# Performance work log

Hardware: AMD Instinct MI355X
Metric: run time of the kernel (lower is better)

Reference implementation:

```python
import jax, jax.numpy as jnp
import numpy as np

BATCH = 32768
NUM_CLASSES = 1024  # balanced binary hierarchy => 10 levels, 1023 internal nodes


def setup_inputs() -> dict:
    key = jax.random.key(0)
    outputs = jax.random.normal(key, (BATCH, NUM_CLASSES), dtype=jnp.float32)
    return {"outputs": outputs}


def reference(outputs) -> jnp.ndarray:
    """SoftEmbeddedDecisionRules.forward for a balanced binary hierarchy.

    For every internal node: child logit = mean of raw logits over the child's
    leaf (class) set, softmax over the node's children, then multiply each
    class's running probability by the prob of the branch containing it.
    With a balanced binary tree over C classes, level l has 2^l nodes, each
    child covering a contiguous block of C / 2^(l+1) classes, so the per-node
    Python loop of the original collapses into one reshape+mean+softmax per
    level (log2(C) fused passes total).
    """
    B, C = outputs.shape
    depth = C.bit_length() - 1  # log2(C), static
    class_probs = jnp.ones((B, C), dtype=outputs.dtype)
    for level in range(depth):
        n_nodes = 1 << level
        seg = C // (2 * n_nodes)  # classes per child subtree
        # node logits: mean of raw logits over each child's class block
        node_logits = outputs.reshape(B, n_nodes, 2, seg).mean(axis=-1)  # [B, n, 2]
        probs = jax.nn.softmax(node_logits, axis=-1)  # softmax over children
        # scatter-multiply child prob onto every class in that child's subtree
        expanded = jnp.broadcast_to(probs[..., None], (B, n_nodes, 2, seg)).reshape(B, C)
        class_probs = class_probs * expanded
    return class_probs
```

## Files before the change

kernel.cpp:

```cpp
#include <hip/hip_runtime.h>


#define C 1024

typedef float f4 __attribute__((ext_vector_type(4)));

__device__ __forceinline__ float sigd(float d) {
    return 1.0f / (1.0f + __expf(d));
}

__global__ __launch_bounds__(256) void hier_softmax_kernel(
    const float* __restrict__ in, float* __restrict__ out, int B) {
    const int lane = threadIdx.x & 63;
    const int waveId = (blockIdx.x * blockDim.x + threadIdx.x) >> 6;
    const int nWaves = (gridDim.x * blockDim.x) >> 6;

    for (int row = waveId; row < B; row += nWaves) {
        const f4* __restrict__ rowp = (const f4*)(in + (size_t)row * C);

        f4 v[4];
#pragma unroll
        for (int q = 0; q < 4; ++q) v[q] = rowp[q * 64 + lane];

        float pA[4], pB[4], p8[4], S[4], common[4];
#pragma unroll
        for (int q = 0; q < 4; ++q) {
            pA[q] = sigd(v[q].y - v[q].x);
            pB[q] = sigd(v[q].w - v[q].z);
            const float s2a = v[q].x + v[q].y;
            const float s2b = v[q].z + v[q].w;
            p8[q] = sigd((s2b - s2a) * 0.5f);
            S[q] = s2a + s2b;
            common[q] = 1.0f;
        }

        float inv = 0.25f;
#pragma unroll
        for (int m = 1; m <= 32; m <<= 1) {
#pragma unroll
            for (int q = 0; q < 4; ++q) {
                const float sib = __shfl_xor(S[q], m, 64);
                common[q] *= sigd((sib - S[q]) * inv);
                S[q] += sib;
            }
            inv *= 0.5f;
        }
        const float topL = sigd(((S[2] + S[3]) - (S[0] + S[1])) * (1.0f / 512.0f));
        const float pq01 = sigd((S[1] - S[0]) * (1.0f / 256.0f));
        const float pq23 = sigd((S[3] - S[2]) * (1.0f / 256.0f));
        const float lvl01[4] = {topL * pq01, topL * (1.0f - pq01),
                                (1.0f - topL) * pq23, (1.0f - topL) * (1.0f - pq23)};

        f4* __restrict__ orow = (f4*)(out + (size_t)row * C);
#pragma unroll
        for (int q = 0; q < 4; ++q) {
            const float cm = common[q] * lvl01[q];
            const float cl = cm * p8[q];
            const float cr = cm * (1.0f - p8[q]);
            f4 o;
            o.x = cl * pA[q];
            o.y = cl * (1.0f - pA[q]);
            o.z = cr * pB[q];
            o.w = cr * (1.0f - pB[q]);
            __builtin_nontemporal_store(o, orow + q * 64 + lane);
        }
    }
}

extern "C" void kernel_launch(void* const* d_in, const int* in_sizes, int n_in,
                              void* d_out, int out_size, void* d_ws, size_t ws_size,
                              hipStream_t stream) {
    const float* in = (const float*)d_in[0];
    float* out = (float*)d_out;
    const int B = in_sizes[0] / C;
    hier_softmax_kernel<<<2048, 256, 0, stream>>>(in, out, B);
}
```

Baseline: 231.5 us.

## Give each lane a contiguous 16-float block and prefetch the next row

Each lane now loads 16 contiguous floats (four adjacent float4s) instead of strided float4s. The lower four tree levels are then resolved inside the lane, so each row needs a single 6-step shuffle reduction instead of four. The next row's data is loaded before the current row is computed, so memory latency overlaps with compute, and the launch bounds request 4 waves per SIMD. The 64-byte-per-lane access pattern may coalesce worse than the previous lane-strided float4 loads, and the prefetch buffer raises register use.

Result: slower. 363.7 us (+57.1%).

```diff
diff --git a/kernel.cpp b/kernel.cpp
--- a/kernel.cpp
+++ b/kernel.cpp
@@ -9,61 +9,98 @@
     return 1.0f / (1.0f + __expf(d));
 }
 
-__global__ __launch_bounds__(256) void hier_softmax_kernel(
+__global__ __launch_bounds__(256, 4) void hier_softmax_kernel(
     const float* __restrict__ in, float* __restrict__ out, int B) {
     const int lane = threadIdx.x & 63;
     const int waveId = (blockIdx.x * blockDim.x + threadIdx.x) >> 6;
     const int nWaves = (gridDim.x * blockDim.x) >> 6;
 
-    for (int row = waveId; row < B; row += nWaves) {
-        const f4* __restrict__ rowp = (const f4*)(in + (size_t)row * C);
+    int row = waveId;
+    if (row >= B) return;
 
-        f4 v[4];
+    f4 v[4];
+    {
+        const f4* rowp = (const f4*)(in + (size_t)row * C);
 #pragma unroll
-        for (int q = 0; q < 4; ++q) v[q] = rowp[q * 64 + lane];
+        for (int j = 0; j < 4; ++j) v[j] = rowp[lane * 4 + j];
+    }
 
-        float pA[4], pB[4], p8[4], S[4], common[4];
+    while (row < B) {
+        const int nrow = row + nWaves;
+        f4 vn[4];
+        if (nrow < B) {
+            const f4* np = (const f4*)(in + (size_t)nrow * C);
 #pragma unroll
-        for (int q = 0; q < 4; ++q) {
-            pA[q] = sigd(v[q].y - v[q].x);
-            pB[q] = sigd(v[q].w - v[q].z);
-            const float s2a = v[q].x + v[q].y;
-            const float s2b = v[q].z + v[q].w;
-            p8[q] = sigd((s2b - s2a) * 0.5f);
-            S[q] = s2a + s2b;
-            common[q] = 1.0f;
+            for (int j = 0; j < 4; ++j) vn[j] = np[lane * 4 + j];
         }
 
-        float inv = 0.25f;
+        float x[16];
+#pragma unroll
+        for (int j = 0; j < 4; ++j) {
+            x[4 * j + 0] = v[j].x; x[4 * j + 1] = v[j].y;
+            x[4 * j + 2] = v[j].z; x[4 * j + 3] = v[j].w;
+        }
+
+        float p1[8], s2[8];
+#pragma unroll
+        for (int k = 0; k < 8; ++k) {
+            p1[k] = sigd(x[2 * k + 1] - x[2 * k]);
+            s2[k] = x[2 * k] + x[2 * k + 1];
+        }
+        float p2[4], s4[4];
+#pragma unroll
+        for (int k = 0; k < 4; ++k) {
+            p2[k] = sigd((s2[2 * k + 1] - s2[2 * k]) * 0.5f);
+            s4[k] = s2[2 * k] + s2[2 * k + 1];
+        }
+        float p4[2], s8[2];
+#pragma unroll
+        for (int k = 0; k < 2; ++k) {
+            p4[k] = sigd((s4[2 * k + 1] - s4[2 * k]) * 0.25f);
+            s8[k] = s4[2 * k] + s4[2 * k + 1];
+        }
+        const float p8 = sigd((s8[1] - s8[0]) * 0.125f);
+        float S = s8[0] + s8[1];
+
+        float common = 1.0f;
+        float inv = 0.0625f;
 #pragma unroll
         for (int m = 1; m <= 32; m <<= 1) {
-#pragma unroll
-            for (int q = 0; q < 4; ++q) {
-                const float sib = __shfl_xor(S[q], m, 64);
-                common[q] *= sigd((sib - S[q]) * inv);
-                S[q] += sib;
-            }
+            const float sib = __shfl_xor(S, m, 64);
+            common *= sigd((sib - S) * inv);
+            S += sib;
             inv *= 0.5f;
         }
-        const float topL = sigd(((S[2] + S[3]) - (S[0] + S[1])) * (1.0f / 512.0f));
-        const float pq01 = sigd((S[1] - S[0]) * (1.0f / 256.0f));
-        const float pq23 = sigd((S[3] - S[2]) * (1.0f / 256.0f));
-        const float lvl01[4] = {topL * pq01, topL * (1.0f - pq01),
-                                (1.0f - topL) * pq23, (1.0f - topL) * (1.0f - pq23)};
 
-        f4* __restrict__ orow = (f4*)(out + (size_t)row * C);
+        float c8[2], c4[4], c2[8];
+        c8[0] = common * p8;
+        c8[1] = common - c8[0];
 #pragma unroll
-        for (int q = 0; q < 4; ++q) {
-            const float cm = common[q] * lvl01[q];
-            const float cl = cm * p8[q];
-            const float cr = cm * (1.0f - p8[q]);
+        for (int k = 0; k < 2; ++k) {
+            c4[2 * k] = c8[k] * p4[k];
+            c4[2 * k + 1] = c8[k] - c4[2 * k];
+        }
+#pragma unroll
+        for (int k = 0; k < 4; ++k) {
+            c2[2 * k] = c4[k] * p2[k];
+            c2[2 * k + 1] = c4[k] - c2[2 * k];
+        }
+
+        f4* orow = (f4*)(out + (size_t)row * C);
+#pragma unroll
+        for (int j = 0; j < 4; ++j) {
+            const int k0 = 2 * j, k1 = 2 * j + 1;
             f4 o;
-            o.x = cl * pA[q];
-            o.y = cl * (1.0f - pA[q]);
-            o.z = cr * pB[q];
-            o.w = cr * (1.0f - pB[q]);
-            __builtin_nontemporal_store(o, orow + q * 64 + lane);
+            o.x = c2[k0] * p1[k0];
+            o.y = c2[k0] - o.x;
+            o.z = c2[k1] * p1[k1];
+            o.w = c2[k1] - o.z;
+            __builtin_nontemporal_store(o, orow + lane * 4 + j);
         }
+
+        row = nrow;
+#pragma unroll
+        for (int j = 0; j < 4; ++j) v[j] = vn[j];
     }
 }
 
```
